# Kernel optimization log

Hardware: AMD Instinct MI355X
Metric: run time of the kernel (lower is better)

Reference implementation:

```python
import math
import jax, jax.numpy as jnp
import numpy as np

B, S, D, H = 4, 2048, 1024, 16
DK = D // H
THETA = 10000.0


def _rope(xh, pos):
    # xh: [B, H, S, DK], pos: [S]
    half = jnp.arange(0, DK, 2, dtype=jnp.float32) / DK
    inv_freq = THETA ** (-half)                      # [DK/2]
    ang = pos.astype(jnp.float32)[:, None] * inv_freq  # [S, DK/2]
    cos, sin = jnp.cos(ang).astype(xh.dtype), jnp.sin(ang).astype(xh.dtype)
    x1, x2 = xh[..., 0::2], xh[..., 1::2]
    r1 = x1 * cos - x2 * sin
    r2 = x1 * sin + x2 * cos
    return jnp.stack([r1, r2], axis=-1).reshape(xh.shape)


def setup_inputs() -> dict:
    key = jax.random.key(0)
    kx, kq, kk, kv, ko = jax.random.split(key, 5)
    std = 0.02
    x = jax.random.normal(kx, (B, S, D), jnp.float32)
    wq = jax.random.normal(kq, (D, D), jnp.float32) * std
    wk = jax.random.normal(kk, (D, D), jnp.float32) * std
    wv = jax.random.normal(kv, (D, D), jnp.float32) * std
    wo = jax.random.normal(ko, (D, D), jnp.float32) * std
    token_positions = jnp.arange(S, dtype=jnp.int32)
    return {"x": x, "wq": wq, "wk": wk, "wv": wv, "wo": wo,
            "token_positions": token_positions}


def reference(x, wq, wk, wv, wo, token_positions):
    # bias-free linear projections: y = x @ W^T (torch Linear convention)
    q = x @ wq.T
    k = x @ wk.T
    v = x @ wv.T
    # split heads: [B, S, D] -> [B, H, S, DK]
    to_heads = lambda t: t.reshape(B, S, H, DK).transpose(0, 2, 1, 3)
    qh, kh, vh = to_heads(q), to_heads(k), to_heads(v)
    qh = _rope(qh, token_positions)
    kh = _rope(kh, token_positions)
    scores = jnp.einsum('bhqd,bhkd->bhqk', qh, kh) / math.sqrt(DK)
    causal = jnp.tril(jnp.ones((S, S), dtype=bool))
    scores = jnp.where(causal, scores, -jnp.inf)
    attn = jax.nn.softmax(scores, axis=-1)
    out = jnp.einsum('bhqk,bhkd->bhqd', attn, vh)       # [B, H, S, DK]
    out = out.transpose(0, 2, 1, 3).reshape(B, S, D)    # merge heads
    return out @ wo.T
```

## Files before the change

kernel.cpp:

```cpp
#include <hip/hip_runtime.h>

#define B_ 4
#define S_ 2048
#define D_ 1024
#define H_ 16
#define DK_ 64
#define M_ (B_*S_)
#define K_ D_
#define N_ D_
#define NSTEP 32

typedef unsigned short u16;
typedef unsigned int u32;
typedef __bf16 bf16x8 __attribute__((ext_vector_type(8)));
typedef float f32x4 __attribute__((ext_vector_type(4)));
typedef u32 u32x4v __attribute__((ext_vector_type(4)));

#define EXP2F(x) __builtin_amdgcn_exp2f(x)

__device__ __forceinline__ u16 f2bf(float f) {
    u32 u = __builtin_bit_cast(u32, f);
    u += 0x7fff + ((u >> 16) & 1);
    return (u16)(u >> 16);
}
__device__ __forceinline__ float bf2f(u16 h) {
    u32 u = ((u32)h) << 16;
    return __builtin_bit_cast(float, u);
}
__device__ __forceinline__ u32 pack_trunc(float a, float b) {
    return (__builtin_bit_cast(u32, a) >> 16) | (__builtin_bit_cast(u32, b) & 0xffff0000u);
}

#define GLDS16(g, l) __builtin_amdgcn_global_load_lds( \
    (__attribute__((address_space(1))) void*)(g),      \
    (__attribute__((address_space(3))) void*)(l), 16, 0, 0)

__global__ __launch_bounds__(256) void cvt_all(
    const float* __restrict__ x,
    const float* __restrict__ w0, const float* __restrict__ w1,
    const float* __restrict__ w2, const float* __restrict__ w3,
    u16* __restrict__ xb,
    u16* __restrict__ o0, u16* __restrict__ o1,
    u16* __restrict__ o2, u16* __restrict__ o3) {
    const size_t i = (size_t)blockIdx.x * 256 + threadIdx.x;
    const float* in;
    u16* out;
    size_t off;
    if (i < 2097152) {
        in = x; out = xb; off = i;
    } else {
        const size_t j = i - 2097152;
        const int wi = (int)(j >> 18);
        off = j & 262143;
        in  = (wi == 0) ? w0 : (wi == 1) ? w1 : (wi == 2) ? w2 : w3;
        out = (wi == 0) ? o0 : (wi == 1) ? o1 : (wi == 2) ? o2 : o3;
    }
    const float4 f = *(const float4*)(in + off * 4);
    u32 p0 = (u32)f2bf(f.x) | ((u32)f2bf(f.y) << 16);
    u32 p1 = (u32)f2bf(f.z) | ((u32)f2bf(f.w) << 16);
    *(uint2*)(out + off * 4) = make_uint2(p0, p1);
}

template <int MODE>
__device__ __forceinline__ void gemm_tile3(const u16* __restrict__ A,
                                           const u16* __restrict__ Bm,
                                           void* __restrict__ Cv,
                                           int m0, int n0,
                                           u16* __restrict__ As,
                                           u16* __restrict__ Bs) {
    const int tid  = threadIdx.x;
    const int wave = tid >> 6, lane = tid & 63;
    const int wm = wave & 1, wn = wave >> 1;
    const int quad = lane >> 4, mcol = lane & 15;

    const int c0 = wave, c1 = wave + 4;
    const int r0 = c0 * 16 + (lane >> 2), r1 = c1 * 16 + (lane >> 2);
    const int kb = (((lane & 3) ^ ((lane >> 3) & 3)) * 8);
    const u16* ga0 = A  + (size_t)(m0 + r0) * K_ + kb;
    const u16* ga1 = A  + (size_t)(m0 + r1) * K_ + kb;
    const u16* gb0 = Bm + (size_t)(n0 + r0) * K_ + kb;
    const u16* gb1 = Bm + (size_t)(n0 + r1) * K_ + kb;
    const int lo0 = c0 * 512, lo1 = c1 * 512;
    const int rsw = ((mcol >> 1) & 3);

    f32x4 acc[4][4];
#pragma unroll
    for (int i = 0; i < 4; i++)
#pragma unroll
        for (int j = 0; j < 4; j++) acc[i][j] = f32x4{0.f, 0.f, 0.f, 0.f};

    GLDS16(ga0, As + lo0); GLDS16(ga1, As + lo1);
    GLDS16(gb0, Bs + lo0); GLDS16(gb1, Bs + lo1);
    ga0 += 32; ga1 += 32; gb0 += 32; gb1 += 32;
    GLDS16(ga0, As + 4096 + lo0); GLDS16(ga1, As + 4096 + lo1);
    GLDS16(gb0, Bs + 4096 + lo0); GLDS16(gb1, Bs + 4096 + lo1);
    ga0 += 32; ga1 += 32; gb0 += 32; gb1 += 32;

    int cur = 0, tgt = 2;
    for (int t = 0; t < NSTEP; ++t) {
        if (t < NSTEP - 1) asm volatile("s_waitcnt vmcnt(4)" ::: "memory");
        else               asm volatile("s_waitcnt vmcnt(0)" ::: "memory");
        asm volatile("s_waitcnt lgkmcnt(0)" ::: "memory");
        __builtin_amdgcn_s_barrier();

        if (t < NSTEP - 2) {
            u16* at = As + tgt * 4096;
            u16* bt = Bs + tgt * 4096;
            GLDS16(ga0, at + lo0); GLDS16(ga1, at + lo1);
            GLDS16(gb0, bt + lo0); GLDS16(gb1, bt + lo1);
            ga0 += 32; ga1 += 32; gb0 += 32; gb1 += 32;
        }

        const u16* Ab = As + cur * 4096;
        const u16* Bb = Bs + cur * 4096;
        bf16x8 af[4], bfr[4];
#pragma unroll
        for (int i = 0; i < 4; i++) {
            af[i]  = *(const bf16x8*)&Ab[(wm * 64 + i * 16 + mcol) * 32 + (quad ^ rsw) * 8];
            bfr[i] = *(const bf16x8*)&Bb[(wn * 64 + i * 16 + mcol) * 32 + (quad ^ rsw) * 8];
        }
        __builtin_amdgcn_s_setprio(1);
#pragma unroll
        for (int i = 0; i < 4; i++)
#pragma unroll
            for (int j = 0; j < 4; j++)
                acc[i][j] = __builtin_amdgcn_mfma_f32_16x16x32_bf16(
                    af[i], bfr[j], acc[i][j], 0, 0, 0);
        __builtin_amdgcn_s_setprio(0);

        cur = (cur == 2) ? 0 : cur + 1;
        tgt = (tgt == 2) ? 0 : tgt + 1;
    }

#pragma unroll
    for (int i = 0; i < 4; i++) {
        const int row = m0 + wm * 64 + i * 16 + quad * 4;
#pragma unroll
        for (int j = 0; j < 4; j++) {
            const int col = n0 + wn * 64 + j * 16 + mcol;
            if constexpr (MODE == 2) {
                const int hh = col >> 6, dd = col & 63;
                const int bb = row >> 11, ss = row & 2047;
                const u32 lo = (u32)f2bf(acc[i][j][0]) | ((u32)f2bf(acc[i][j][1]) << 16);
                const u32 hi = (u32)f2bf(acc[i][j][2]) | ((u32)f2bf(acc[i][j][3]) << 16);
                *(uint2*)((u16*)Cv + ((size_t)((bb * H_ + hh) * DK_ + dd)) * S_ + ss) =
                    make_uint2(lo, hi);
            } else {
#pragma unroll
                for (int r = 0; r < 4; r++) {
                    if constexpr (MODE == 1)
                        ((float*)Cv)[(size_t)(row + r) * N_ + col] = acc[i][j][r];
                    else
                        ((u16*)Cv)[(size_t)(row + r) * N_ + col] = f2bf(acc[i][j][r]);
                }
            }
        }
    }
}

__global__ __launch_bounds__(256) void gemm_qkv_kernel(
    const u16* __restrict__ x,
    const u16* __restrict__ wq, const u16* __restrict__ wk,
    const u16* __restrict__ wv,
    u16* __restrict__ q, u16* __restrict__ k, u16* __restrict__ vt) {
    __shared__ u16 As[3 * 4096];
    __shared__ u16 Bs[3 * 4096];
    const int flat = blockIdx.x;
    const int w = (flat & 7) * 192 + (flat >> 3);
    const int my = w / 24;
    const int rem = w - my * 24;
    const int z = rem >> 3, nx = rem & 7;
    const int m0 = my * 128, n0 = nx * 128;
    if (z == 2) {
        gemm_tile3<2>(x, wv, vt, m0, n0, As, Bs);
    } else {
        const u16* Bm = z ? wk : wq;
        u16* C        = z ? k  : q;
        gemm_tile3<0>(x, Bm, C, m0, n0, As, Bs);
    }
}

__global__ __launch_bounds__(256) void gemm_out_kernel(
    const u16* __restrict__ o, const u16* __restrict__ wo, float* __restrict__ out) {
    __shared__ u16 As[2][128 * 32];
    __shared__ u16 Bs[2][128 * 32];
    const int flat = blockIdx.x;
    const int w = (flat & 7) * 64 + (flat >> 3);
    const int m0 = (w >> 3) * 128, n0 = (w & 7) * 128;

    const int tid  = threadIdx.x;
    const int wave = tid >> 6, lane = tid & 63;
    const int wm = wave & 1, wn = wave >> 1;
    const int quad = lane >> 4, mcol = lane & 15;

    const int c0 = wave, c1 = wave + 4;
    const int r0 = c0 * 16 + (lane >> 2), r1 = c1 * 16 + (lane >> 2);
    const int kb = (((lane & 3) ^ ((lane >> 3) & 3)) * 8);
    const u16* ga0 = o  + (size_t)(m0 + r0) * K_ + kb;
    const u16* ga1 = o  + (size_t)(m0 + r1) * K_ + kb;
    const u16* gb0 = wo + (size_t)(n0 + r0) * K_ + kb;
    const u16* gb1 = wo + (size_t)(n0 + r1) * K_ + kb;
    const int lo0 = c0 * 512, lo1 = c1 * 512;
    const int rsw = ((mcol >> 1) & 3);

    f32x4 acc[4][4];
#pragma unroll
    for (int i = 0; i < 4; i++)
#pragma unroll
        for (int j = 0; j < 4; j++) acc[i][j] = f32x4{0.f, 0.f, 0.f, 0.f};

    GLDS16(ga0, &As[0][lo0]); GLDS16(ga1, &As[0][lo1]);
    GLDS16(gb0, &Bs[0][lo0]); GLDS16(gb1, &Bs[0][lo1]);
    ga0 += 32; ga1 += 32; gb0 += 32; gb1 += 32;
    __syncthreads();

    for (int kt = 0; kt < K_; kt += 32) {
        const int cur = (kt >> 5) & 1;
        if (kt + 32 < K_) {
            const int nxt = cur ^ 1;
            GLDS16(ga0, &As[nxt][lo0]); GLDS16(ga1, &As[nxt][lo1]);
            GLDS16(gb0, &Bs[nxt][lo0]); GLDS16(gb1, &Bs[nxt][lo1]);
            ga0 += 32; ga1 += 32; gb0 += 32; gb1 += 32;
        }

        bf16x8 af[4], bfr[4];
#pragma unroll
        for (int i = 0; i < 4; i++) {
            af[i]  = *(const bf16x8*)&As[cur][(wm * 64 + i * 16 + mcol) * 32 + (quad ^ rsw) * 8];
            bfr[i] = *(const bf16x8*)&Bs[cur][(wn * 64 + i * 16 + mcol) * 32 + (quad ^ rsw) * 8];
        }
        __builtin_amdgcn_s_setprio(1);
#pragma unroll
        for (int i = 0; i < 4; i++)
#pragma unroll
            for (int j = 0; j < 4; j++)
                acc[i][j] = __builtin_amdgcn_mfma_f32_16x16x32_bf16(
                    af[i], bfr[j], acc[i][j], 0, 0, 0);
        __builtin_amdgcn_s_setprio(0);

        __syncthreads();
    }

#pragma unroll
    for (int i = 0; i < 4; i++) {
        const int row = m0 + wm * 64 + i * 16 + quad * 4;
#pragma unroll
        for (int j = 0; j < 4; j++) {
            const int col = n0 + wn * 64 + j * 16 + mcol;
#pragma unroll
            for (int r = 0; r < 4; r++)
                out[(size_t)(row + r) * N_ + col] = acc[i][j][r];
        }
    }
}

__global__ __launch_bounds__(256) void rope_qk(u16* __restrict__ q,
                                               u16* __restrict__ k,
                                               const int* __restrict__ pos) {
    const int idx = blockIdx.x * 256 + threadIdx.x;
    const int seg = idx & 3;
    const int h = (idx >> 2) & (H_ - 1);
    const int s = (idx >> 6) & (S_ - 1);
    const int b = idx >> 17;
    const float p = (float)pos[s];
    const float QSC = 0.18033688011112042f;
    const size_t off = ((size_t)(b * S_ + s)) * D_ + h * DK_ + seg * 16;

    u32 qa[8], ka[8];
    *(uint4*)&qa[0] = *(const uint4*)(q + off);
    *(uint4*)&qa[4] = *(const uint4*)(q + off + 8);
    *(uint4*)&ka[0] = *(const uint4*)(k + off);
    *(uint4*)&ka[4] = *(const uint4*)(k + off + 8);
#pragma unroll
    for (int w = 0; w < 8; w++) {
        const int i = seg * 8 + w;
        const float inv = exp2f((float)i * (-13.287712379549449f / 32.f));
        const float ang = p * inv;
        float sn, cs;
        __sincosf(ang, &sn, &cs);
        {
            const float x1 = bf2f((u16)(qa[w] & 0xffff));
            const float x2 = bf2f((u16)(qa[w] >> 16));
            qa[w] = (u32)f2bf((x1 * cs - x2 * sn) * QSC) |
                    ((u32)f2bf((x1 * sn + x2 * cs) * QSC) << 16);
        }
        {
            const float x1 = bf2f((u16)(ka[w] & 0xffff));
            const float x2 = bf2f((u16)(ka[w] >> 16));
            ka[w] = (u32)f2bf(x1 * cs - x2 * sn) |
                    ((u32)f2bf(x1 * sn + x2 * cs) << 16);
        }
    }
    *(uint4*)(q + off)     = *(uint4*)&qa[0];
    *(uint4*)(q + off + 8) = *(uint4*)&qa[4];
    *(uint4*)(k + off)     = *(uint4*)&ka[0];
    *(uint4*)(k + off + 8) = *(uint4*)&ka[4];
}

__global__ __launch_bounds__(256) void attn_kernel(
    const u16* __restrict__ q, const u16* __restrict__ k,
    const u16* __restrict__ vt, u16* __restrict__ o) {
    __shared__ u16 Ks[64 * 64];
    __shared__ u16 Vs[64 * 64];

    const int tid = threadIdx.x, wave = tid >> 6, lane = tid & 63;
    const int flat = blockIdx.x;
    const int qp = flat >> 6;
    const int h = flat & (H_ - 1);
    const int b = (flat >> 4) & 3;
    const int quad = lane >> 4, mcol = lane & 15;
    const int srd = mcol & 7;

    const int rr2 = tid >> 2, cc2 = tid & 3;
    const int sw = rr2 & 7;
    const int so0 = rr2 * 64 + (((cc2 * 2)     ^ sw) << 3);
    const int so1 = rr2 * 64 + (((cc2 * 2 + 1) ^ sw) << 3);
    const int prr = (rr2 & 35) | ((rr2 & 12) << 1) | ((rr2 & 16) >> 2);
    const int ch2 = cc2 * 16;
    const u16* krow = k + ((size_t)(b * S_ + prr)) * D_ + h * DK_ + ch2;
    const u16* vrow = vt + ((size_t)((b * H_ + h) * DK_ + rr2)) * S_ + ch2;

    u32x4v onesw;
    onesw[0] = onesw[1] = onesw[2] = onesw[3] = 0x3F803F80u;
    const bf16x8 onesf = __builtin_bit_cast(bf16x8, onesw);

    for (int pass = 0; pass < 2; pass++) {
        const int qt = pass ? (15 - qp) : qp;
        const int q0 = qt * 128;
        const int wq0 = q0 + wave * 32;
        const int jmax = 2 * qt + 1;

        bf16x8 qf[2][2];
#pragma unroll
        for (int g = 0; g < 2; g++) {
            const u16* qs = q + ((size_t)(b * S_ + wq0 + g * 16 + mcol)) * D_ + h * DK_ + quad * 8;
            qf[g][0] = *(const bf16x8*)qs;
            qf[g][1] = *(const bf16x8*)(qs + 32);
        }

        float m[2] = {-1e30f, -1e30f};
        f32x4 lacc[2];
        f32x4 oacc[2][4];
#pragma unroll
        for (int g = 0; g < 2; g++) {
            lacc[g] = f32x4{0.f, 0.f, 0.f, 0.f};
#pragma unroll
            for (int dn = 0; dn < 4; dn++) oacc[g][dn] = f32x4{0.f, 0.f, 0.f, 0.f};
        }

        uint4 kr0 = *(const uint4*)(krow);
        uint4 kr1 = *(const uint4*)(krow + 8);
        uint4 vr0 = *(const uint4*)(vrow);
        uint4 vr1 = *(const uint4*)(vrow + 8);

        for (int j = 0; j <= jmax; j++) {
            __syncthreads();
            *(uint4*)&Ks[so0] = kr0;
            *(uint4*)&Ks[so1] = kr1;
            *(uint4*)&Vs[so0] = vr0;
            *(uint4*)&Vs[so1] = vr1;
            __syncthreads();

            if (j < jmax) {
                kr0 = *(const uint4*)(krow + (size_t)(j + 1) * 64 * D_);
                kr1 = *(const uint4*)(krow + (size_t)(j + 1) * 64 * D_ + 8);
                vr0 = *(const uint4*)(vrow + (j + 1) * 64);
                vr1 = *(const uint4*)(vrow + (j + 1) * 64 + 8);
            }

            if (j * 64 > wq0 + 31) continue;

            f32x4 st[2][4];
            __builtin_amdgcn_s_setprio(1);
#pragma unroll
            for (int n = 0; n < 4; n++) {
                const u16* kl = &Ks[(n * 16 + mcol) * 64];
                bf16x8 kf0 = *(const bf16x8*)&kl[(quad ^ srd) << 3];
                bf16x8 kf1 = *(const bf16x8*)&kl[((quad | 4) ^ srd) << 3];
                f32x4 z0 = f32x4{0.f, 0.f, 0.f, 0.f};
                z0 = __builtin_amdgcn_mfma_f32_16x16x32_bf16(kf0, qf[0][0], z0, 0, 0, 0);
                z0 = __builtin_amdgcn_mfma_f32_16x16x32_bf16(kf1, qf[0][1], z0, 0, 0, 0);
                st[0][n] = z0;
                f32x4 z1 = f32x4{0.f, 0.f, 0.f, 0.f};
                z1 = __builtin_amdgcn_mfma_f32_16x16x32_bf16(kf0, qf[1][0], z1, 0, 0, 0);
                z1 = __builtin_amdgcn_mfma_f32_16x16x32_bf16(kf1, qf[1][1], z1, 0, 0, 0);
                st[1][n] = z1;
            }
            __builtin_amdgcn_s_setprio(0);

            if (j * 64 + 63 > wq0) {
#pragma unroll
                for (int g = 0; g < 2; g++) {
                    const int qg = wq0 + g * 16 + mcol;
#pragma unroll
                    for (int n = 0; n < 4; n++) {
                        const int tb = j * 64 + ((n >> 1) << 5) + ((n & 1) << 2) + quad * 8;
#pragma unroll
                        for (int r = 0; r < 4; r++)
                            if (tb + r > qg) st[g][n][r] = -1e30f;
                    }
                }
            }

#pragma unroll
            for (int g = 0; g < 2; g++) {
                float mx = st[g][0][0];
#pragma unroll
                for (int n = 0; n < 4; n++)
#pragma unroll
                    for (int r = 0; r < 4; r++) mx = fmaxf(mx, st[g][n][r]);
                mx = fmaxf(mx, __shfl_xor(mx, 16));
                mx = fmaxf(mx, __shfl_xor(mx, 32));
                const bool need = !__all(mx <= m[g] + 8.f);
                if (need) {
                    const float mnew = fmaxf(m[g], mx);
                    const float al = EXP2F(m[g] - mnew);
                    m[g] = mnew;
                    float alphaT[4];
#pragma unroll
                    for (int r = 0; r < 4; r++) alphaT[r] = __shfl(al, quad * 4 + r);
#pragma unroll
                    for (int dn = 0; dn < 4; dn++)
#pragma unroll
                        for (int r = 0; r < 4; r++) oacc[g][dn][r] *= alphaT[r];
#pragma unroll
                    for (int r = 0; r < 4; r++) lacc[g][r] *= alphaT[r];
                }
#pragma unroll
                for (int n = 0; n < 4; n++)
#pragma unroll
                    for (int r = 0; r < 4; r++)
                        st[g][n][r] = EXP2F(st[g][n][r] - m[g]);
            }

            bf16x8 pf[2][2];
#pragma unroll
            for (int g = 0; g < 2; g++) {
                u32x4v w0, w1;
                w0[0] = pack_trunc(st[g][0][0], st[g][0][1]);
                w0[1] = pack_trunc(st[g][0][2], st[g][0][3]);
                w0[2] = pack_trunc(st[g][1][0], st[g][1][1]);
                w0[3] = pack_trunc(st[g][1][2], st[g][1][3]);
                w1[0] = pack_trunc(st[g][2][0], st[g][2][1]);
                w1[1] = pack_trunc(st[g][2][2], st[g][2][3]);
                w1[2] = pack_trunc(st[g][3][0], st[g][3][1]);
                w1[3] = pack_trunc(st[g][3][2], st[g][3][3]);
                pf[g][0] = __builtin_bit_cast(bf16x8, w0);
                pf[g][1] = __builtin_bit_cast(bf16x8, w1);
            }

            __builtin_amdgcn_s_setprio(1);
#pragma unroll
            for (int g = 0; g < 2; g++) {
                lacc[g] = __builtin_amdgcn_mfma_f32_16x16x32_bf16(pf[g][0], onesf, lacc[g], 0, 0, 0);
                lacc[g] = __builtin_amdgcn_mfma_f32_16x16x32_bf16(pf[g][1], onesf, lacc[g], 0, 0, 0);
            }
#pragma unroll
            for (int dn = 0; dn < 4; dn++) {
                const u16* vl = &Vs[(dn * 16 + mcol) * 64];
                bf16x8 vf0 = *(const bf16x8*)&vl[(quad ^ srd) << 3];
                bf16x8 vf1 = *(const bf16x8*)&vl[((quad | 4) ^ srd) << 3];
#pragma unroll
                for (int g = 0; g < 2; g++) {
                    oacc[g][dn] = __builtin_amdgcn_mfma_f32_16x16x32_bf16(pf[g][0], vf0, oacc[g][dn], 0, 0, 0);
                    oacc[g][dn] = __builtin_amdgcn_mfma_f32_16x16x32_bf16(pf[g][1], vf1, oacc[g][dn], 0, 0, 0);
                }
            }
            __builtin_amdgcn_s_setprio(0);
        }

#pragma unroll
        for (int g = 0; g < 2; g++) {
            float linv[4];
#pragma unroll
            for (int r = 0; r < 4; r++) linv[r] = 1.f / lacc[g][r];
#pragma unroll
            for (int dn = 0; dn < 4; dn++)
#pragma unroll
                for (int r = 0; r < 4; r++) {
                    const int row = wq0 + g * 16 + quad * 4 + r;
                    o[((size_t)(b * S_ + row)) * D_ + h * DK_ + dn * 16 + mcol] =
                        f2bf(oacc[g][dn][r] * linv[r]);
                }
        }
    }
}

extern "C" void kernel_launch(void* const* d_in, const int* in_sizes, int n_in,
                              void* d_out, int out_size, void* d_ws, size_t ws_size,
                              hipStream_t stream) {
    const float* x  = (const float*)d_in[0];
    const float* wq = (const float*)d_in[1];
    const float* wk = (const float*)d_in[2];
    const float* wv = (const float*)d_in[3];
    const float* wo = (const float*)d_in[4];
    const int*   tp = (const int*)d_in[5];
    float* out = (float*)d_out;

    u16* ws = (u16*)d_ws;
    const size_t NE = (size_t)M_ * D_;
    const size_t WE = (size_t)N_ * K_;
    u16* xb  = ws;
    u16* wqb = ws + NE;
    u16* wkb = wqb + WE;
    u16* wvb = wkb + WE;
    u16* wob = wvb + WE;
    u16* qb  = wob + WE;
    u16* kb  = qb + NE;
    u16* vtb = (u16*)d_out;
    u16* ob  = xb;

    dim3 blk(256);
    cvt_all<<<dim3(12288), blk, 0, stream>>>(x, wq, wk, wv, wo,
                                             xb, wqb, wkb, wvb, wob);

    gemm_qkv_kernel<<<dim3(3 * (M_ / 128) * (N_ / 128)), blk, 0, stream>>>(
        xb, wqb, wkb, wvb, qb, kb, vtb);
    rope_qk<<<dim3((B_ * S_ * H_ * 4) / 256), blk, 0, stream>>>(qb, kb, tp);
    attn_kernel<<<dim3((S_ / 128 / 2) * H_ * B_), blk, 0, stream>>>(qb, kb, vtb, ob);
    gemm_out_kernel<<<dim3((M_ / 128) * (N_ / 128)), blk, 0, stream>>>(ob, wob, out);
}
```

Baseline: 255.4 us.

## Rewrite QKV GEMM with 256x256 tiles, 512 threads and split-phase MFMA scheduling

The fused QKV projection GEMM moves from 128x128 tiles (256 threads, triple-buffered K=32 steps) to 256x256 tiles computed by 512 threads over double-buffered K=64 stages. Each wave computes 128x64 and interleaves its LDS fragment loads with four MFMA phases separated by barriers, with a new XOR swizzle and XCD-aware block mapping. The aim is higher arithmetic intensity and fewer global and LDS loads per flop. In exchange it uses more LDS and registers per block (128 KB LDS for two buffers) and launches only 384 blocks, which may underfill the GPU.

```diff
diff --git a/kernel.cpp b/kernel.cpp
--- a/kernel.cpp
+++ b/kernel.cpp
@@ -9,6 +9,7 @@
 #define K_ D_
 #define N_ D_
 #define NSTEP 32
+#define NT 16
 
 typedef unsigned short u16;
 typedef unsigned int u32;
@@ -34,6 +35,12 @@
 #define GLDS16(g, l) __builtin_amdgcn_global_load_lds( \
     (__attribute__((address_space(1))) void*)(g),      \
     (__attribute__((address_space(3))) void*)(l), 16, 0, 0)
+
+__device__ __forceinline__ void barrier_fence() {
+    asm volatile("" ::: "memory");
+    __builtin_amdgcn_s_barrier();
+    asm volatile("" ::: "memory");
+}
 
 __global__ __launch_bounds__(256) void cvt_all(
     const float* __restrict__ x,
@@ -62,121 +69,175 @@
 }
 
 template <int MODE>
-__device__ __forceinline__ void gemm_tile3(const u16* __restrict__ A,
-                                           const u16* __restrict__ Bm,
-                                           void* __restrict__ Cv,
-                                           int m0, int n0,
-                                           u16* __restrict__ As,
-                                           u16* __restrict__ Bs) {
+__device__ __forceinline__ void gemm_tile256(const u16* __restrict__ A,
+                                             const u16* __restrict__ Bm,
+                                             void* __restrict__ Cv,
+                                             int m0, int n0,
+                                             u16* __restrict__ As,
+                                             u16* __restrict__ Bs) {
     const int tid  = threadIdx.x;
     const int wave = tid >> 6, lane = tid & 63;
-    const int wm = wave & 1, wn = wave >> 1;
+    const int wm = wave >> 2, wn = wave & 3;
     const int quad = lane >> 4, mcol = lane & 15;
 
-    const int c0 = wave, c1 = wave + 4;
-    const int r0 = c0 * 16 + (lane >> 2), r1 = c1 * 16 + (lane >> 2);
-    const int kb = (((lane & 3) ^ ((lane >> 3) & 3)) * 8);
-    const u16* ga0 = A  + (size_t)(m0 + r0) * K_ + kb;
-    const u16* ga1 = A  + (size_t)(m0 + r1) * K_ + kb;
-    const u16* gb0 = Bm + (size_t)(n0 + r0) * K_ + kb;
-    const u16* gb1 = Bm + (size_t)(n0 + r1) * K_ + kb;
-    const int lo0 = c0 * 512, lo1 = c1 * 512;
-    const int rsw = ((mcol >> 1) & 3);
-
-    f32x4 acc[4][4];
-#pragma unroll
-    for (int i = 0; i < 4; i++)
-#pragma unroll
-        for (int j = 0; j < 4; j++) acc[i][j] = f32x4{0.f, 0.f, 0.f, 0.f};
-
-    GLDS16(ga0, As + lo0); GLDS16(ga1, As + lo1);
-    GLDS16(gb0, Bs + lo0); GLDS16(gb1, Bs + lo1);
-    ga0 += 32; ga1 += 32; gb0 += 32; gb1 += 32;
-    GLDS16(ga0, As + 4096 + lo0); GLDS16(ga1, As + 4096 + lo1);
-    GLDS16(gb0, Bs + 4096 + lo0); GLDS16(gb1, Bs + 4096 + lo1);
-    ga0 += 32; ga1 += 32; gb0 += 32; gb1 += 32;
-
-    int cur = 0, tgt = 2;
-    for (int t = 0; t < NSTEP; ++t) {
-        if (t < NSTEP - 1) asm volatile("s_waitcnt vmcnt(4)" ::: "memory");
-        else               asm volatile("s_waitcnt vmcnt(0)" ::: "memory");
-        asm volatile("s_waitcnt lgkmcnt(0)" ::: "memory");
-        __builtin_amdgcn_s_barrier();
-
-        if (t < NSTEP - 2) {
-            u16* at = As + tgt * 4096;
-            u16* bt = Bs + tgt * 4096;
-            GLDS16(ga0, at + lo0); GLDS16(ga1, at + lo1);
-            GLDS16(gb0, bt + lo0); GLDS16(gb1, bt + lo1);
-            ga0 += 32; ga1 += 32; gb0 += 32; gb1 += 32;
-        }
-
-        const u16* Ab = As + cur * 4096;
-        const u16* Bb = Bs + cur * 4096;
-        bf16x8 af[4], bfr[4];
-#pragma unroll
-        for (int i = 0; i < 4; i++) {
-            af[i]  = *(const bf16x8*)&Ab[(wm * 64 + i * 16 + mcol) * 32 + (quad ^ rsw) * 8];
-            bfr[i] = *(const bf16x8*)&Bb[(wn * 64 + i * 16 + mcol) * 32 + (quad ^ rsw) * 8];
-        }
+    const int srow = wave * 8 + (lane >> 3);
+    const int csrc = (lane & 7) ^ ((lane >> 3) & 7);
+    const u16* gA = A  + (size_t)(m0 + srow) * K_ + csrc * 8;
+    const u16* gB = Bm + (size_t)(n0 + srow) * K_ + csrc * 8;
+    const int ldst = wave * 512;
+
+    const int rx = mcol & 7;
+    const int abase = (wm * 128 + mcol) * 64;
+    const int bbase = (wn * 64 + mcol) * 64;
+    const int cA0 = ((0 * 4 + quad) ^ rx) * 8;
+    const int cA1 = ((1 * 4 + quad) ^ rx) * 8;
+
+    f32x4 acc[8][4];
+#pragma unroll
+    for (int f = 0; f < 8; f++)
+#pragma unroll
+        for (int j = 0; j < 4; j++) acc[f][j] = f32x4{0.f, 0.f, 0.f, 0.f};
+
+#define STAGE_T(bufA, bufB, koff) do {                                       \
+    _Pragma("unroll") for (int i = 0; i < 4; ++i) {                          \
+        GLDS16(gA + (koff) + (size_t)i * 64 * K_, (bufA) + ldst + i * 4096); \
+        GLDS16(gB + (koff) + (size_t)i * 64 * K_, (bufB) + ldst + i * 4096); \
+    } } while (0)
+
+    STAGE_T(As, Bs, 0);
+    STAGE_T(As + 16384, Bs + 16384, 64);
+    asm volatile("s_waitcnt vmcnt(8)" ::: "memory");
+    barrier_fence();
+
+    bf16x8 af[4][2], bfr[4][2];
+
+    for (int t = 0; t < NT; ++t) {
+        const u16* Ab = As + ((t & 1) ? 16384 : 0);
+        const u16* Bb = Bs + ((t & 1) ? 16384 : 0);
+
+#pragma unroll
+        for (int f = 0; f < 4; f++) {
+            af[f][0] = *(const bf16x8*)&Ab[abase + f * 1024 + cA0];
+            af[f][1] = *(const bf16x8*)&Ab[abase + f * 1024 + cA1];
+        }
+#pragma unroll
+        for (int j = 0; j < 2; j++) {
+            bfr[j][0] = *(const bf16x8*)&Bb[bbase + j * 1024 + cA0];
+            bfr[j][1] = *(const bf16x8*)&Bb[bbase + j * 1024 + cA1];
+        }
+        barrier_fence();
         __builtin_amdgcn_s_setprio(1);
 #pragma unroll
-        for (int i = 0; i < 4; i++)
-#pragma unroll
-            for (int j = 0; j < 4; j++)
-                acc[i][j] = __builtin_amdgcn_mfma_f32_16x16x32_bf16(
-                    af[i], bfr[j], acc[i][j], 0, 0, 0);
+        for (int f = 0; f < 4; f++)
+#pragma unroll
+            for (int j = 0; j < 2; j++) {
+                acc[f][j] = __builtin_amdgcn_mfma_f32_16x16x32_bf16(af[f][0], bfr[j][0], acc[f][j], 0, 0, 0);
+                acc[f][j] = __builtin_amdgcn_mfma_f32_16x16x32_bf16(af[f][1], bfr[j][1], acc[f][j], 0, 0, 0);
+            }
         __builtin_amdgcn_s_setprio(0);
-
-        cur = (cur == 2) ? 0 : cur + 1;
-        tgt = (tgt == 2) ? 0 : tgt + 1;
-    }
-
-#pragma unroll
-    for (int i = 0; i < 4; i++) {
-        const int row = m0 + wm * 64 + i * 16 + quad * 4;
+        barrier_fence();
+
+#pragma unroll
+        for (int j = 2; j < 4; j++) {
+            bfr[j][0] = *(const bf16x8*)&Bb[bbase + j * 1024 + cA0];
+            bfr[j][1] = *(const bf16x8*)&Bb[bbase + j * 1024 + cA1];
+        }
+        barrier_fence();
+        __builtin_amdgcn_s_setprio(1);
+#pragma unroll
+        for (int f = 0; f < 4; f++)
+#pragma unroll
+            for (int j = 2; j < 4; j++) {
+                acc[f][j] = __builtin_amdgcn_mfma_f32_16x16x32_bf16(af[f][0], bfr[j][0], acc[f][j], 0, 0, 0);
+                acc[f][j] = __builtin_amdgcn_mfma_f32_16x16x32_bf16(af[f][1], bfr[j][1], acc[f][j], 0, 0, 0);
+            }
+        __builtin_amdgcn_s_setprio(0);
+        barrier_fence();
+
+#pragma unroll
+        for (int f = 0; f < 4; f++) {
+            af[f][0] = *(const bf16x8*)&Ab[abase + (f + 4) * 1024 + cA0];
+            af[f][1] = *(const bf16x8*)&Ab[abase + (f + 4) * 1024 + cA1];
+        }
+        barrier_fence();
+        __builtin_amdgcn_s_setprio(1);
+#pragma unroll
+        for (int f = 0; f < 4; f++)
+#pragma unroll
+            for (int j = 2; j < 4; j++) {
+                acc[f + 4][j] = __builtin_amdgcn_mfma_f32_16x16x32_bf16(af[f][0], bfr[j][0], acc[f + 4][j], 0, 0, 0);
+                acc[f + 4][j] = __builtin_amdgcn_mfma_f32_16x16x32_bf16(af[f][1], bfr[j][1], acc[f + 4][j], 0, 0, 0);
+            }
+        __builtin_amdgcn_s_setprio(0);
+        barrier_fence();
+
+        if (t + 2 < NT) {
+            u16* sa = As + ((t & 1) ? 16384 : 0);
+            u16* sb = Bs + ((t & 1) ? 16384 : 0);
+            STAGE_T(sa, sb, (size_t)(t + 2) * 64);
+        }
+        __builtin_amdgcn_s_setprio(1);
+#pragma unroll
+        for (int f = 0; f < 4; f++)
+#pragma unroll
+            for (int j = 0; j < 2; j++) {
+                acc[f + 4][j] = __builtin_amdgcn_mfma_f32_16x16x32_bf16(af[f][0], bfr[j][0], acc[f + 4][j], 0, 0, 0);
+                acc[f + 4][j] = __builtin_amdgcn_mfma_f32_16x16x32_bf16(af[f][1], bfr[j][1], acc[f + 4][j], 0, 0, 0);
+            }
+        __builtin_amdgcn_s_setprio(0);
+
+        if (t < NT - 1) {
+            if (t < NT - 2) asm volatile("s_waitcnt vmcnt(8)" ::: "memory");
+            else            asm volatile("s_waitcnt vmcnt(0)" ::: "memory");
+            barrier_fence();
+        }
+    }
+#undef STAGE_T
+
+#pragma unroll
+    for (int f = 0; f < 8; f++) {
+        const int row = m0 + wm * 128 + f * 16 + quad * 4;
 #pragma unroll
         for (int j = 0; j < 4; j++) {
             const int col = n0 + wn * 64 + j * 16 + mcol;
             if constexpr (MODE == 2) {
                 const int hh = col >> 6, dd = col & 63;
                 const int bb = row >> 11, ss = row & 2047;
-                const u32 lo = (u32)f2bf(acc[i][j][0]) | ((u32)f2bf(acc[i][j][1]) << 16);
-                const u32 hi = (u32)f2bf(acc[i][j][2]) | ((u32)f2bf(acc[i][j][3]) << 16);
+                const u32 lo = (u32)f2bf(acc[f][j][0]) | ((u32)f2bf(acc[f][j][1]) << 16);
+                const u32 hi = (u32)f2bf(acc[f][j][2]) | ((u32)f2bf(acc[f][j][3]) << 16);
                 *(uint2*)((u16*)Cv + ((size_t)((bb * H_ + hh) * DK_ + dd)) * S_ + ss) =
                     make_uint2(lo, hi);
             } else {
 #pragma unroll
-                for (int r = 0; r < 4; r++) {
-                    if constexpr (MODE == 1)
-                        ((float*)Cv)[(size_t)(row + r) * N_ + col] = acc[i][j][r];
-                    else
-                        ((u16*)Cv)[(size_t)(row + r) * N_ + col] = f2bf(acc[i][j][r]);
-                }
-            }
-        }
-    }
-}
-
-__global__ __launch_bounds__(256) void gemm_qkv_kernel(
+                for (int r = 0; r < 4; r++)
+                    ((u16*)Cv)[(size_t)(row + r) * N_ + col] = f2bf(acc[f][j][r]);
+            }
+        }
+    }
+}
+
+__global__ __launch_bounds__(512, 2) void gemm_qkv_kernel(
     const u16* __restrict__ x,
     const u16* __restrict__ wq, const u16* __restrict__ wk,
     const u16* __restrict__ wv,
     u16* __restrict__ q, u16* __restrict__ k, u16* __restrict__ vt) {
-    __shared__ u16 As[3 * 4096];
-    __shared__ u16 Bs[3 * 4096];
+    __shared__ u16 As[2 * 16384];
+    __shared__ u16 Bs[2 * 16384];
     const int flat = blockIdx.x;
-    const int w = (flat & 7) * 192 + (flat >> 3);
-    const int my = w / 24;
-    const int rem = w - my * 24;
-    const int z = rem >> 3, nx = rem & 7;
-    const int m0 = my * 128, n0 = nx * 128;
+    const int xcd = flat & 7;
+    const int loc = flat >> 3;
+    const int myl = loc / 12;
+    const int rem = loc - myl * 12;
+    const int z  = rem >> 2;
+    const int nx = rem & 3;
+    const int m0 = (xcd * 4 + myl) * 256;
+    const int n0 = nx * 256;
     if (z == 2) {
-        gemm_tile3<2>(x, wv, vt, m0, n0, As, Bs);
+        gemm_tile256<2>(x, wv, vt, m0, n0, As, Bs);
     } else {
         const u16* Bm = z ? wk : wq;
         u16* C        = z ? k  : q;
-        gemm_tile3<0>(x, Bm, C, m0, n0, As, Bs);
+        gemm_tile256<0>(x, Bm, C, m0, n0, As, Bs);
     }
 }
 
@@ -514,7 +575,7 @@
     cvt_all<<<dim3(12288), blk, 0, stream>>>(x, wq, wk, wv, wo,
                                              xb, wqb, wkb, wvb, wob);
 
-    gemm_qkv_kernel<<<dim3(3 * (M_ / 128) * (N_ / 128)), blk, 0, stream>>>(
+    gemm_qkv_kernel<<<dim3(3 * (M_ / 256) * (N_ / 256)), dim3(512), 0, stream>>>(
         xb, wqb, wkb, wvb, qb, kb, vtb);
     rope_qk<<<dim3((B_ * S_ * H_ * 4) / 256), blk, 0, stream>>>(qb, kb, tp);
     attn_kernel<<<dim3((S_ / 128 / 2) * H_ * B_), blk, 0, stream>>>(qb, kb, vtb, ob);
```

Result: slower. 265.2 us (+3.8%).

## Split attention into 64-row query tiles with 2-wave blocks, heaviest tiles first

Applied to the files above, without the earlier changes.

The attention kernel moves from 256-thread blocks, each handling a pair of 128-row query tiles (folded for causal balance), to 128-thread blocks that each handle one 64-row query tile. Blocks are ordered so the longest causal tiles launch first. Each thread now stages four 16-byte K/V chunks instead of two, and masking runs only on the diagonal block. This quadruples the grid and gives finer scheduling granularity. In exchange, each loaded K/V tile is shared by half as many query rows and there are more block launches.

```diff
diff --git a/kernel.cpp b/kernel.cpp
--- a/kernel.cpp
+++ b/kernel.cpp
@@ -297,7 +297,7 @@
     *(uint4*)(k + off + 8) = *(uint4*)&ka[4];
 }
 
-__global__ __launch_bounds__(256) void attn_kernel(
+__global__ __launch_bounds__(128) void attn_kernel(
     const u16* __restrict__ q, const u16* __restrict__ k,
     const u16* __restrict__ vt, u16* __restrict__ o) {
     __shared__ u16 Ks[64 * 64];
@@ -305,18 +305,23 @@
 
     const int tid = threadIdx.x, wave = tid >> 6, lane = tid & 63;
     const int flat = blockIdx.x;
-    const int qp = flat >> 6;
+    const int qt = 31 - (flat >> 6);
     const int h = flat & (H_ - 1);
     const int b = (flat >> 4) & 3;
     const int quad = lane >> 4, mcol = lane & 15;
     const int srd = mcol & 7;
-
-    const int rr2 = tid >> 2, cc2 = tid & 3;
+    const int q0 = qt * 64;
+    const int wq0 = q0 + wave * 32;
+    const int jmax = qt;
+
+    const int rr2 = tid >> 1, cc2 = tid & 1;
     const int sw = rr2 & 7;
-    const int so0 = rr2 * 64 + (((cc2 * 2)     ^ sw) << 3);
-    const int so1 = rr2 * 64 + (((cc2 * 2 + 1) ^ sw) << 3);
+    int so[4];
+#pragma unroll
+    for (int t = 0; t < 4; t++)
+        so[t] = rr2 * 64 + (((cc2 * 4 + t) ^ sw) << 3);
     const int prr = (rr2 & 35) | ((rr2 & 12) << 1) | ((rr2 & 16) >> 2);
-    const int ch2 = cc2 * 16;
+    const int ch2 = cc2 * 32;
     const u16* krow = k + ((size_t)(b * S_ + prr)) * D_ + h * DK_ + ch2;
     const u16* vrow = vt + ((size_t)((b * H_ + h) * DK_ + rr2)) * S_ + ch2;
 
@@ -324,165 +329,160 @@
     onesw[0] = onesw[1] = onesw[2] = onesw[3] = 0x3F803F80u;
     const bf16x8 onesf = __builtin_bit_cast(bf16x8, onesw);
 
-    for (int pass = 0; pass < 2; pass++) {
-        const int qt = pass ? (15 - qp) : qp;
-        const int q0 = qt * 128;
-        const int wq0 = q0 + wave * 32;
-        const int jmax = 2 * qt + 1;
-
-        bf16x8 qf[2][2];
-#pragma unroll
-        for (int g = 0; g < 2; g++) {
-            const u16* qs = q + ((size_t)(b * S_ + wq0 + g * 16 + mcol)) * D_ + h * DK_ + quad * 8;
-            qf[g][0] = *(const bf16x8*)qs;
-            qf[g][1] = *(const bf16x8*)(qs + 32);
-        }
-
-        float m[2] = {-1e30f, -1e30f};
-        f32x4 lacc[2];
-        f32x4 oacc[2][4];
-#pragma unroll
-        for (int g = 0; g < 2; g++) {
-            lacc[g] = f32x4{0.f, 0.f, 0.f, 0.f};
-#pragma unroll
-            for (int dn = 0; dn < 4; dn++) oacc[g][dn] = f32x4{0.f, 0.f, 0.f, 0.f};
-        }
-
-        uint4 kr0 = *(const uint4*)(krow);
-        uint4 kr1 = *(const uint4*)(krow + 8);
-        uint4 vr0 = *(const uint4*)(vrow);
-        uint4 vr1 = *(const uint4*)(vrow + 8);
-
-        for (int j = 0; j <= jmax; j++) {
-            __syncthreads();
-            *(uint4*)&Ks[so0] = kr0;
-            *(uint4*)&Ks[so1] = kr1;
-            *(uint4*)&Vs[so0] = vr0;
-            *(uint4*)&Vs[so1] = vr1;
-            __syncthreads();
-
-            if (j < jmax) {
-                kr0 = *(const uint4*)(krow + (size_t)(j + 1) * 64 * D_);
-                kr1 = *(const uint4*)(krow + (size_t)(j + 1) * 64 * D_ + 8);
-                vr0 = *(const uint4*)(vrow + (j + 1) * 64);
-                vr1 = *(const uint4*)(vrow + (j + 1) * 64 + 8);
+    bf16x8 qf[2][2];
+#pragma unroll
+    for (int g = 0; g < 2; g++) {
+        const u16* qs = q + ((size_t)(b * S_ + wq0 + g * 16 + mcol)) * D_ + h * DK_ + quad * 8;
+        qf[g][0] = *(const bf16x8*)qs;
+        qf[g][1] = *(const bf16x8*)(qs + 32);
+    }
+
+    float m[2] = {-1e30f, -1e30f};
+    f32x4 lacc[2];
+    f32x4 oacc[2][4];
+#pragma unroll
+    for (int g = 0; g < 2; g++) {
+        lacc[g] = f32x4{0.f, 0.f, 0.f, 0.f};
+#pragma unroll
+        for (int dn = 0; dn < 4; dn++) oacc[g][dn] = f32x4{0.f, 0.f, 0.f, 0.f};
+    }
+
+    uint4 kr[4], vr[4];
+#pragma unroll
+    for (int t = 0; t < 4; t++) {
+        kr[t] = *(const uint4*)(krow + t * 8);
+        vr[t] = *(const uint4*)(vrow + t * 8);
+    }
+
+    for (int j = 0; j <= jmax; j++) {
+        __syncthreads();
+#pragma unroll
+        for (int t = 0; t < 4; t++) {
+            *(uint4*)&Ks[so[t]] = kr[t];
+            *(uint4*)&Vs[so[t]] = vr[t];
+        }
+        __syncthreads();
+
+        if (j < jmax) {
+#pragma unroll
+            for (int t = 0; t < 4; t++) {
+                kr[t] = *(const uint4*)(krow + (size_t)(j + 1) * 64 * D_ + t * 8);
+                vr[t] = *(const uint4*)(vrow + (j + 1) * 64 + t * 8);
             }
-
-            if (j * 64 > wq0 + 31) continue;
-
-            f32x4 st[2][4];
-            __builtin_amdgcn_s_setprio(1);
-#pragma unroll
-            for (int n = 0; n < 4; n++) {
-                const u16* kl = &Ks[(n * 16 + mcol) * 64];
-                bf16x8 kf0 = *(const bf16x8*)&kl[(quad ^ srd) << 3];
-                bf16x8 kf1 = *(const bf16x8*)&kl[((quad | 4) ^ srd) << 3];
-                f32x4 z0 = f32x4{0.f, 0.f, 0.f, 0.f};
-                z0 = __builtin_amdgcn_mfma_f32_16x16x32_bf16(kf0, qf[0][0], z0, 0, 0, 0);
-                z0 = __builtin_amdgcn_mfma_f32_16x16x32_bf16(kf1, qf[0][1], z0, 0, 0, 0);
-                st[0][n] = z0;
-                f32x4 z1 = f32x4{0.f, 0.f, 0.f, 0.f};
-                z1 = __builtin_amdgcn_mfma_f32_16x16x32_bf16(kf0, qf[1][0], z1, 0, 0, 0);
-                z1 = __builtin_amdgcn_mfma_f32_16x16x32_bf16(kf1, qf[1][1], z1, 0, 0, 0);
-                st[1][n] = z1;
-            }
-            __builtin_amdgcn_s_setprio(0);
-
-            if (j * 64 + 63 > wq0) {
-#pragma unroll
-                for (int g = 0; g < 2; g++) {
-                    const int qg = wq0 + g * 16 + mcol;
-#pragma unroll
-                    for (int n = 0; n < 4; n++) {
-                        const int tb = j * 64 + ((n >> 1) << 5) + ((n & 1) << 2) + quad * 8;
-#pragma unroll
-                        for (int r = 0; r < 4; r++)
-                            if (tb + r > qg) st[g][n][r] = -1e30f;
-                    }
+        }
+
+        f32x4 st[2][4];
+        __builtin_amdgcn_s_setprio(1);
+#pragma unroll
+        for (int n = 0; n < 4; n++) {
+            const u16* kl = &Ks[(n * 16 + mcol) * 64];
+            bf16x8 kf0 = *(const bf16x8*)&kl[(quad ^ srd) << 3];
+            bf16x8 kf1 = *(const bf16x8*)&kl[((quad | 4) ^ srd) << 3];
+            f32x4 z0 = f32x4{0.f, 0.f, 0.f, 0.f};
+            z0 = __builtin_amdgcn_mfma_f32_16x16x32_bf16(kf0, qf[0][0], z0, 0, 0, 0);
+            z0 = __builtin_amdgcn_mfma_f32_16x16x32_bf16(kf1, qf[0][1], z0, 0, 0, 0);
+            st[0][n] = z0;
+            f32x4 z1 = f32x4{0.f, 0.f, 0.f, 0.f};
+            z1 = __builtin_amdgcn_mfma_f32_16x16x32_bf16(kf0, qf[1][0], z1, 0, 0, 0);
+            z1 = __builtin_amdgcn_mfma_f32_16x16x32_bf16(kf1, qf[1][1], z1, 0, 0, 0);
+            st[1][n] = z1;
+        }
+        __builtin_amdgcn_s_setprio(0);
+
+        if (j == jmax) {
+#pragma unroll
+            for (int g = 0; g < 2; g++) {
+                const int qg = wq0 + g * 16 + mcol;
+#pragma unroll
+                for (int n = 0; n < 4; n++) {
+                    const int tb = j * 64 + ((n >> 1) << 5) + ((n & 1) << 2) + quad * 8;
+#pragma unroll
+                    for (int r = 0; r < 4; r++)
+                        if (tb + r > qg) st[g][n][r] = -1e30f;
                 }
             }
-
+        }
+
+#pragma unroll
+        for (int g = 0; g < 2; g++) {
+            float mx = st[g][0][0];
+#pragma unroll
+            for (int n = 0; n < 4; n++)
+#pragma unroll
+                for (int r = 0; r < 4; r++) mx = fmaxf(mx, st[g][n][r]);
+            mx = fmaxf(mx, __shfl_xor(mx, 16));
+            mx = fmaxf(mx, __shfl_xor(mx, 32));
+            const bool need = !__all(mx <= m[g] + 8.f);
+            if (need) {
+                const float mnew = fmaxf(m[g], mx);
+                const float al = EXP2F(m[g] - mnew);
+                m[g] = mnew;
+                float alphaT[4];
+#pragma unroll
+                for (int r = 0; r < 4; r++) alphaT[r] = __shfl(al, quad * 4 + r);
+#pragma unroll
+                for (int dn = 0; dn < 4; dn++)
+#pragma unroll
+                    for (int r = 0; r < 4; r++) oacc[g][dn][r] *= alphaT[r];
+#pragma unroll
+                for (int r = 0; r < 4; r++) lacc[g][r] *= alphaT[r];
+            }
+#pragma unroll
+            for (int n = 0; n < 4; n++)
+#pragma unroll
+                for (int r = 0; r < 4; r++)
+                    st[g][n][r] = EXP2F(st[g][n][r] - m[g]);
+        }
+
+        bf16x8 pf[2][2];
+#pragma unroll
+        for (int g = 0; g < 2; g++) {
+            u32x4v w0, w1;
+            w0[0] = pack_trunc(st[g][0][0], st[g][0][1]);
+            w0[1] = pack_trunc(st[g][0][2], st[g][0][3]);
+            w0[2] = pack_trunc(st[g][1][0], st[g][1][1]);
+            w0[3] = pack_trunc(st[g][1][2], st[g][1][3]);
+            w1[0] = pack_trunc(st[g][2][0], st[g][2][1]);
+            w1[1] = pack_trunc(st[g][2][2], st[g][2][3]);
+            w1[2] = pack_trunc(st[g][3][0], st[g][3][1]);
+            w1[3] = pack_trunc(st[g][3][2], st[g][3][3]);
+            pf[g][0] = __builtin_bit_cast(bf16x8, w0);
+            pf[g][1] = __builtin_bit_cast(bf16x8, w1);
+        }
+
+        __builtin_amdgcn_s_setprio(1);
+#pragma unroll
+        for (int g = 0; g < 2; g++) {
+            lacc[g] = __builtin_amdgcn_mfma_f32_16x16x32_bf16(pf[g][0], onesf, lacc[g], 0, 0, 0);
+            lacc[g] = __builtin_amdgcn_mfma_f32_16x16x32_bf16(pf[g][1], onesf, lacc[g], 0, 0, 0);
+        }
+#pragma unroll
+        for (int dn = 0; dn < 4; dn++) {
+            const u16* vl = &Vs[(dn * 16 + mcol) * 64];
+            bf16x8 vf0 = *(const bf16x8*)&vl[(quad ^ srd) << 3];
+            bf16x8 vf1 = *(const bf16x8*)&vl[((quad | 4) ^ srd) << 3];
 #pragma unroll
             for (int g = 0; g < 2; g++) {
-                float mx = st[g][0][0];
-#pragma unroll
-                for (int n = 0; n < 4; n++)
-#pragma unroll
-                    for (int r = 0; r < 4; r++) mx = fmaxf(mx, st[g][n][r]);
-                mx = fmaxf(mx, __shfl_xor(mx, 16));
-                mx = fmaxf(mx, __shfl_xor(mx, 32));
-                const bool need = !__all(mx <= m[g] + 8.f);
-                if (need) {
-                    const float mnew = fmaxf(m[g], mx);
-                    const float al = EXP2F(m[g] - mnew);
-                    m[g] = mnew;
-                    float alphaT[4];
-#pragma unroll
-                    for (int r = 0; r < 4; r++) alphaT[r] = __shfl(al, quad * 4 + r);
-#pragma unroll
-                    for (int dn = 0; dn < 4; dn++)
-#pragma unroll
-                        for (int r = 0; r < 4; r++) oacc[g][dn][r] *= alphaT[r];
-#pragma unroll
-                    for (int r = 0; r < 4; r++) lacc[g][r] *= alphaT[r];
-                }
-#pragma unroll
-                for (int n = 0; n < 4; n++)
-#pragma unroll
-                    for (int r = 0; r < 4; r++)
-                        st[g][n][r] = EXP2F(st[g][n][r] - m[g]);
+                oacc[g][dn] = __builtin_amdgcn_mfma_f32_16x16x32_bf16(pf[g][0], vf0, oacc[g][dn], 0, 0, 0);
+                oacc[g][dn] = __builtin_amdgcn_mfma_f32_16x16x32_bf16(pf[g][1], vf1, oacc[g][dn], 0, 0, 0);
             }
-
-            bf16x8 pf[2][2];
-#pragma unroll
-            for (int g = 0; g < 2; g++) {
-                u32x4v w0, w1;
-                w0[0] = pack_trunc(st[g][0][0], st[g][0][1]);
-                w0[1] = pack_trunc(st[g][0][2], st[g][0][3]);
-                w0[2] = pack_trunc(st[g][1][0], st[g][1][1]);
-                w0[3] = pack_trunc(st[g][1][2], st[g][1][3]);
-                w1[0] = pack_trunc(st[g][2][0], st[g][2][1]);
-                w1[1] = pack_trunc(st[g][2][2], st[g][2][3]);
-                w1[2] = pack_trunc(st[g][3][0], st[g][3][1]);
-                w1[3] = pack_trunc(st[g][3][2], st[g][3][3]);
-                pf[g][0] = __builtin_bit_cast(bf16x8, w0);
-                pf[g][1] = __builtin_bit_cast(bf16x8, w1);
+        }
+        __builtin_amdgcn_s_setprio(0);
+    }
+
+#pragma unroll
+    for (int g = 0; g < 2; g++) {
+        float linv[4];
+#pragma unroll
+        for (int r = 0; r < 4; r++) linv[r] = 1.f / lacc[g][r];
+#pragma unroll
+        for (int dn = 0; dn < 4; dn++)
+#pragma unroll
+            for (int r = 0; r < 4; r++) {
+                const int row = wq0 + g * 16 + quad * 4 + r;
+                o[((size_t)(b * S_ + row)) * D_ + h * DK_ + dn * 16 + mcol] =
+                    f2bf(oacc[g][dn][r] * linv[r]);
             }
-
-            __builtin_amdgcn_s_setprio(1);
-#pragma unroll
-            for (int g = 0; g < 2; g++) {
-                lacc[g] = __builtin_amdgcn_mfma_f32_16x16x32_bf16(pf[g][0], onesf, lacc[g], 0, 0, 0);
-                lacc[g] = __builtin_amdgcn_mfma_f32_16x16x32_bf16(pf[g][1], onesf, lacc[g], 0, 0, 0);
-            }
-#pragma unroll
-            for (int dn = 0; dn < 4; dn++) {
-                const u16* vl = &Vs[(dn * 16 + mcol) * 64];
-                bf16x8 vf0 = *(const bf16x8*)&vl[(quad ^ srd) << 3];
-                bf16x8 vf1 = *(const bf16x8*)&vl[((quad | 4) ^ srd) << 3];
-#pragma unroll
-                for (int g = 0; g < 2; g++) {
-                    oacc[g][dn] = __builtin_amdgcn_mfma_f32_16x16x32_bf16(pf[g][0], vf0, oacc[g][dn], 0, 0, 0);
-                    oacc[g][dn] = __builtin_amdgcn_mfma_f32_16x16x32_bf16(pf[g][1], vf1, oacc[g][dn], 0, 0, 0);
-                }
-            }
-            __builtin_amdgcn_s_setprio(0);
-        }
-
-#pragma unroll
-        for (int g = 0; g < 2; g++) {
-            float linv[4];
-#pragma unroll
-            for (int r = 0; r < 4; r++) linv[r] = 1.f / lacc[g][r];
-#pragma unroll
-            for (int dn = 0; dn < 4; dn++)
-#pragma unroll
-                for (int r = 0; r < 4; r++) {
-                    const int row = wq0 + g * 16 + quad * 4 + r;
-                    o[((size_t)(b * S_ + row)) * D_ + h * DK_ + dn * 16 + mcol] =
-                        f2bf(oacc[g][dn][r] * linv[r]);
-                }
-        }
     }
 }
 
@@ -517,6 +517,6 @@
     gemm_qkv_kernel<<<dim3(3 * (M_ / 128) * (N_ / 128)), blk, 0, stream>>>(
         xb, wqb, wkb, wvb, qb, kb, vtb);
     rope_qk<<<dim3((B_ * S_ * H_ * 4) / 256), blk, 0, stream>>>(qb, kb, tp);
-    attn_kernel<<<dim3((S_ / 128 / 2) * H_ * B_), blk, 0, stream>>>(qb, kb, vtb, ob);
+    attn_kernel<<<dim3((S_ / 64) * H_ * B_), dim3(128), 0, stream>>>(qb, kb, vtb, ob);
     gemm_out_kernel<<<dim3((M_ / 128) * (N_ / 128)), blk, 0, stream>>>(ob, wob, out);
 }
```

New measurement: 358.0 us. 40.2% more time.
